# Kernel tuning notes

Hardware: AMD Instinct MI355X
Metric: run time of the kernel (lower is better)

The kernel has to match this reference:

```python
import jax, jax.numpy as jnp
import numpy as np

K_HOPS = 10
ALPHA = 0.1
N_NODES = 50000
N_EDGES = 600000
F_IN = 128
HIDDEN = 64
N_CLASSES = 40


def setup_inputs() -> dict:
    key = jax.random.key(0)
    k1, k2, k3, k4 = jax.random.split(key, 4)
    x = jax.random.normal(k1, (N_NODES, F_IN), dtype=jnp.float32)
    edge_index = jax.random.randint(k2, (2, N_EDGES), 0, N_NODES, dtype=jnp.int32)
    edge_weight = jnp.ones((N_EDGES,), dtype=jnp.float32)
    W1 = jax.random.normal(k3, (F_IN, HIDDEN), dtype=jnp.float32) * (1.0 / np.sqrt(F_IN))
    b1 = jnp.zeros((HIDDEN,), dtype=jnp.float32)
    W2 = jax.random.normal(k4, (HIDDEN, N_CLASSES), dtype=jnp.float32) * (1.0 / np.sqrt(HIDDEN))
    b2 = jnp.zeros((N_CLASSES,), dtype=jnp.float32)
    return {"x": x, "edge_index": edge_index, "edge_weight": edge_weight,
            "W1": W1, "b1": b1, "W2": W2, "b2": b2}


def reference(x, edge_index, edge_weight, W1, b1, W2, b2):
    n = x.shape[0]
    # GCN symmetric normalization with self-loops (tfg gcn cache)
    self_idx = jnp.arange(n, dtype=edge_index.dtype)
    row = jnp.concatenate([edge_index[0], self_idx])
    col = jnp.concatenate([edge_index[1], self_idx])
    w = jnp.concatenate([edge_weight, jnp.ones((n,), dtype=edge_weight.dtype)])
    deg = jax.ops.segment_sum(w, row, num_segments=n)
    dinv = jnp.where(deg > 0, jax.lax.rsqrt(jnp.maximum(deg, 1e-12)), 0.0)
    nw = dinv[row] * w * dinv[col]  # [E+N] normalized edge weights

    def prop(h):
        # h_out[i] = sum_{(i,j)} nw * h[j]
        return jax.ops.segment_sum(h[col] * nw[:, None], row, num_segments=n)

    def step(h, _):
        h_next = prop(h)
        return h_next, None

    # SSGC: out = (1-alpha)/K * sum_{l=1..K} T^l x + alpha * x
    def step_acc(carry, _):
        h, acc = carry
        h_next = prop(h)
        return (h_next, acc + h_next), None

    (_, acc), _ = jax.lax.scan(step_acc, (x, jnp.zeros_like(x)), None, length=K_HOPS)
    h = (1.0 - ALPHA) / K_HOPS * acc + ALPHA * x  # [N, F]

    h = jax.nn.relu(h @ W1 + b1)  # [N, HIDDEN]
    logits = h @ W2 + b2          # [N, N_CLASSES]
    return logits
```

## Files before the change

### kernel.cpp

```cpp
#include <hip/hip_runtime.h>
#include <hip/hip_fp16.h>
#include <math.h>

constexpr int   N   = 50000;
constexpr int   E   = 600000;
constexpr int   FIN = 128;
constexpr int   H   = 64;
constexpr int   C   = 40;
constexpr int   K   = 10;
constexpr float CK  = (1.0f - 0.1f) / 10.0f;
constexpr float AL  = 0.1f;

typedef float v2f __attribute__((ext_vector_type(2)));

__device__ __forceinline__ unsigned pack_fp8x4(float f0, float f1, float f2, float f3) {
    unsigned r = __builtin_amdgcn_cvt_pk_fp8_f32(f0, f1, 0u, false);
    r = __builtin_amdgcn_cvt_pk_fp8_f32(f2, f3, r, true);
    return r;
}

__device__ __forceinline__ float ep_w(unsigned v) {
    return __half2float(__ushort_as_half((unsigned short)(v >> 16)));
}
__device__ __forceinline__ unsigned ep_pack(int c, float w) {
    return (unsigned)(unsigned short)c |
           ((unsigned)__half_as_ushort(__float2half_rn(w)) << 16);
}

__device__ __forceinline__ void accum8(float* s, uint2 v, float w) {
    v2f p0 = __builtin_amdgcn_cvt_pk_f32_fp8(v.x, false);
    v2f p1 = __builtin_amdgcn_cvt_pk_f32_fp8(v.x, true);
    v2f p2 = __builtin_amdgcn_cvt_pk_f32_fp8(v.y, false);
    v2f p3 = __builtin_amdgcn_cvt_pk_f32_fp8(v.y, true);
    s[0] = fmaf(w, p0.x, s[0]); s[1] = fmaf(w, p0.y, s[1]);
    s[2] = fmaf(w, p1.x, s[2]); s[3] = fmaf(w, p1.y, s[3]);
    s[4] = fmaf(w, p2.x, s[4]); s[5] = fmaf(w, p2.y, s[5]);
    s[6] = fmaf(w, p3.x, s[6]); s[7] = fmaf(w, p3.y, s[7]);
}

constexpr int G1N  = 64;
constexpr int XPAD = 132;
__global__ __launch_bounds__(256, 2) void k_gemm1(const float* __restrict__ x,
                                                  const float* __restrict__ W1,
                                                  float* __restrict__ y0,
                                                  unsigned char* __restrict__ y0f8) {
    __shared__ float ws[FIN * H];
    __shared__ float xs[G1N * XPAD];
    const float4* W14 = (const float4*)W1;
    const float4* x4  = (const float4*)x;
    int t = threadIdx.x;
    int node0 = blockIdx.x * G1N;
    for (int i = t; i < FIN * H / 4; i += 256) ((float4*)ws)[i] = W14[i];
    for (int p = 0; p < 8; ++p) {
        int idx = p * 256 + t;
        int n   = idx >> 5;
        int kk  = idx & 31;
        int node = node0 + n;
        float4 v = (node < N) ? x4[(size_t)node * (FIN / 4) + kk]
                              : make_float4(0.f, 0.f, 0.f, 0.f);
        *(float4*)(xs + n * XPAD + kk * 4) = v;
    }
    __syncthreads();
    int nb = (t >> 4) * 4;
    int cb = (t & 15) * 4;
    float a00=0,a01=0,a02=0,a03=0, a10=0,a11=0,a12=0,a13=0;
    float a20=0,a21=0,a22=0,a23=0, a30=0,a31=0,a32=0,a33=0;
#pragma unroll 8
    for (int k = 0; k < FIN; ++k) {
        float4 wv = *(const float4*)(ws + k * H + cb);
        float x0 = xs[(nb + 0) * XPAD + k];
        float x1 = xs[(nb + 1) * XPAD + k];
        float x2 = xs[(nb + 2) * XPAD + k];
        float x3 = xs[(nb + 3) * XPAD + k];
        a00 = fmaf(x0, wv.x, a00); a01 = fmaf(x0, wv.y, a01);
        a02 = fmaf(x0, wv.z, a02); a03 = fmaf(x0, wv.w, a03);
        a10 = fmaf(x1, wv.x, a10); a11 = fmaf(x1, wv.y, a11);
        a12 = fmaf(x1, wv.z, a12); a13 = fmaf(x1, wv.w, a13);
        a20 = fmaf(x2, wv.x, a20); a21 = fmaf(x2, wv.y, a21);
        a22 = fmaf(x2, wv.z, a22); a23 = fmaf(x2, wv.w, a23);
        a30 = fmaf(x3, wv.x, a30); a31 = fmaf(x3, wv.y, a31);
        a32 = fmaf(x3, wv.z, a32); a33 = fmaf(x3, wv.w, a33);
    }
    float4 rows[4] = {make_float4(a00,a01,a02,a03), make_float4(a10,a11,a12,a13),
                      make_float4(a20,a21,a22,a23), make_float4(a30,a31,a32,a33)};
#pragma unroll
    for (int i = 0; i < 4; ++i) {
        int node = node0 + nb + i;
        if (node >= N) break;
        float4 r = rows[i];
        *(float4*)(y0 + (size_t)node * H + cb) = r;
        *(unsigned*)(y0f8 + (size_t)node * H + cb) = pack_fp8x4(r.x, r.y, r.z, r.w);
    }
}

__global__ void k_count(const int* __restrict__ row, int* __restrict__ cnt8) {
    int e = blockIdx.x * blockDim.x + threadIdx.x;
    if (e >= E) return;
    atomicAdd(&cnt8[(size_t)(blockIdx.x & 7) * N + row[e]], 1);
}

__global__ __launch_bounds__(1024) void k_scan_blocks(const int* __restrict__ cnt8,
                                                      int* __restrict__ row_ptr,
                                                      int* __restrict__ bsum) {
    __shared__ int s[1024];
    int gid = blockIdx.x * 1024 + threadIdx.x;
    int v = 0;
    if (gid < N) {
#pragma unroll
        for (int c = 0; c < 8; ++c) v += cnt8[(size_t)c * N + gid];
    }
    s[threadIdx.x] = v;
    __syncthreads();
    for (int off = 1; off < 1024; off <<= 1) {
        int t = (threadIdx.x >= off) ? s[threadIdx.x - off] : 0;
        __syncthreads();
        s[threadIdx.x] += t;
        __syncthreads();
    }
    if (gid < N) row_ptr[gid] = s[threadIdx.x] - v;
    if (threadIdx.x == 1023) bsum[blockIdx.x] = s[1023];
}

__global__ void k_scan_sums(const int* __restrict__ bsum, int* __restrict__ boff, int nb) {
    int lane = threadIdx.x;
    int orig = (lane < nb) ? bsum[lane] : 0;
    int v = orig;
    for (int off = 1; off < 64; off <<= 1) {
        int t = __shfl_up(v, off, 64);
        if (lane >= off) v += t;
    }
    if (lane < nb) boff[lane] = v - orig;
}

__global__ __launch_bounds__(1024) void k_addoff(int* __restrict__ row_ptr,
                                                 const int* __restrict__ boff,
                                                 int* __restrict__ cnt8) {
    int gid = blockIdx.x * 1024 + threadIdx.x;
    if (gid < N) {
        int rp = row_ptr[gid] + boff[blockIdx.x];
        row_ptr[gid] = rp;
        int off = rp;
#pragma unroll
        for (int c = 0; c < 8; ++c) {
            int t = cnt8[(size_t)c * N + gid];
            cnt8[(size_t)c * N + gid] = off;
            off += t;
        }
    }
    if (gid == 0) row_ptr[N] = E;
}

__global__ void k_scatter(const int* __restrict__ row, const int* __restrict__ col,
                          const float* __restrict__ w,
                          int* __restrict__ off8, unsigned* __restrict__ ep) {
    int e = blockIdx.x * blockDim.x + threadIdx.x;
    if (e >= E) return;
    int r = row[e];
    int p = atomicAdd(&off8[(size_t)(blockIdx.x & 7) * N + r], 1);
    ep[p] = ep_pack(col[e], w[e]);
}

__global__ void k_deg_dinv(const unsigned* __restrict__ ep, const int* __restrict__ row_ptr,
                           float* __restrict__ dinv, float* __restrict__ dinv2) {
    int i = blockIdx.x * blockDim.x + threadIdx.x;
    if (i >= N) return;
    float d = 1.0f;
    int e0 = row_ptr[i], e1 = row_ptr[i + 1];
    for (int j = e0; j < e1; ++j) d += ep_w(ep[j]);
    float di = rsqrtf(d);
    dinv[i]  = di;
    dinv2[i] = di * di;
}

__global__ __launch_bounds__(256) void k_norm(unsigned* __restrict__ ep,
                                              const int* __restrict__ row_ptr,
                                              const float* __restrict__ dinv) {
    int node = blockIdx.x * 32 + (threadIdx.x >> 3);
    if (node >= N) return;
    int l = threadIdx.x & 7;
    float dr = dinv[node];
    int e0 = row_ptr[node], e1 = row_ptr[node + 1];
    for (int j = e0 + l; j < e1; j += 8) {
        unsigned v = ep[j];
        int c = v & 0xFFFFu;
        ep[j] = ep_pack(c, ep_w(v) * dr * dinv[c]);
    }
}

constexpr int HSP = 68;
template <bool WRITE_H, bool ACC_INIT, bool FINAL>
__global__ __launch_bounds__(256) void k_prop(const uint2* __restrict__ hin,
                                              uint2* __restrict__ hout,
                                              __half* __restrict__ acch,
                                              const float* __restrict__ dinv2,
                                              const int* __restrict__ row_ptr,
                                              const unsigned* __restrict__ ep,
                                              const float4* __restrict__ y04,
                                              const float* __restrict__ b1,
                                              const float* __restrict__ W2,
                                              const float* __restrict__ b2,
                                              float* __restrict__ out) {
    extern __shared__ float smem[];
    float* w2s = smem;
    float* hs  = smem + H * C;
    float* b2s = hs + 32 * HSP;
    float* b1s = b2s + C;
    int t = threadIdx.x;
    if (FINAL) {
        for (int i = t; i < H * C; i += 256) w2s[i] = W2[i];
        if (t < C) b2s[t] = b2[t];
        if (t < H) b1s[t] = b1[t];
        __syncthreads();
    }
    int lane = t & 63;
    int nib  = (t >> 6) * 8 + (lane >> 3);
    int l    = lane & 7;
    int node = blockIdx.x * 32 + nib;
    bool nv  = node < N;
    int nodec = nv ? node : N - 1;
    int start = row_ptr[nodec];
    int deg   = nv ? (row_ptr[nodec + 1] - start) : 0;
    int md = deg;
#pragma unroll
    for (int off = 8; off <= 32; off <<= 1) md = max(md, __shfl_xor(md, off, 64));
    float s[8];
#pragma unroll
    for (int i = 0; i < 8; ++i) s[i] = 0.f;
    for (int j = 0; j < md; j += 4) {
        bool a0 = j < deg, a1 = j + 1 < deg, a2 = j + 2 < deg, a3 = j + 3 < deg;
        unsigned e0 = ep[a0 ? start + j     : 0];
        unsigned e1 = ep[a1 ? start + j + 1 : 0];
        unsigned e2 = ep[a2 ? start + j + 2 : 0];
        unsigned e3 = ep[a3 ? start + j + 3 : 0];
        uint2 v0 = hin[(size_t)(e0 & 0xFFFFu) * 8 + l];
        uint2 v1 = hin[(size_t)(e1 & 0xFFFFu) * 8 + l];
        uint2 v2 = hin[(size_t)(e2 & 0xFFFFu) * 8 + l];
        uint2 v3 = hin[(size_t)(e3 & 0xFFFFu) * 8 + l];
        accum8(s, v0, a0 ? ep_w(e0) : 0.0f);
        accum8(s, v1, a1 ? ep_w(e1) : 0.0f);
        accum8(s, v2, a2 ? ep_w(e2) : 0.0f);
        accum8(s, v3, a3 ? ep_w(e3) : 0.0f);
    }
    if (nv) {
        size_t base = (size_t)nodec * 8 + l;
        accum8(s, hin[base], dinv2[nodec]);
        if (WRITE_H) {
            uint2 o;
            o.x = pack_fp8x4(s[0], s[1], s[2], s[3]);
            o.y = pack_fp8x4(s[4], s[5], s[6], s[7]);
            hout[base] = o;
        }
        uint4* ap = (uint4*)(acch + (size_t)nodec * H + l * 8);
        if (FINAL) {
            uint4 old = *ap;
            const unsigned* u = (const unsigned*)&old;
#pragma unroll
            for (int d = 0; d < 4; ++d) {
                float2 f = __half22float2(*(__half2*)&u[d]);
                s[2*d+0] += f.x; s[2*d+1] += f.y;
            }
            float4 ya = y04[(size_t)nodec * (H / 4) + 2 * l];
            float4 yb = y04[(size_t)nodec * (H / 4) + 2 * l + 1];
            const float* bp = b1s + l * 8;
            float* hp = hs + nib * HSP + l * 8;
            hp[0] = fmaxf(fmaf(CK, s[0], fmaf(AL, ya.x, bp[0])), 0.f);
            hp[1] = fmaxf(fmaf(CK, s[1], fmaf(AL, ya.y, bp[1])), 0.f);
            hp[2] = fmaxf(fmaf(CK, s[2], fmaf(AL, ya.z, bp[2])), 0.f);
            hp[3] = fmaxf(fmaf(CK, s[3], fmaf(AL, ya.w, bp[3])), 0.f);
            hp[4] = fmaxf(fmaf(CK, s[4], fmaf(AL, yb.x, bp[4])), 0.f);
            hp[5] = fmaxf(fmaf(CK, s[5], fmaf(AL, yb.y, bp[5])), 0.f);
            hp[6] = fmaxf(fmaf(CK, s[6], fmaf(AL, yb.z, bp[6])), 0.f);
            hp[7] = fmaxf(fmaf(CK, s[7], fmaf(AL, yb.w, bp[7])), 0.f);
        } else {
            if (!ACC_INIT) {
                uint4 old = *ap;
                const unsigned* u = (const unsigned*)&old;
#pragma unroll
                for (int d = 0; d < 4; ++d) {
                    float2 f = __half22float2(*(__half2*)&u[d]);
                    s[2*d+0] += f.x; s[2*d+1] += f.y;
                }
            }
            uint4 nvp;
            unsigned* u = (unsigned*)&nvp;
#pragma unroll
            for (int d = 0; d < 4; ++d) {
                __half2 h = __floats2half2_rn(s[2*d+0], s[2*d+1]);
                u[d] = *(unsigned*)&h;
            }
            *ap = nvp;
        }
    }
    if (FINAL) {
        __syncthreads();
        int node0 = blockIdx.x * 32;
        for (int o = t; o < 32 * C; o += 256) {
            int nl = o / C, c = o % C;
            int n2 = node0 + nl;
            if (n2 >= N) continue;
            float v = b2s[c];
            const float* hr = &hs[nl * HSP];
#pragma unroll
            for (int k = 0; k < H; ++k) v = fmaf(hr[k], w2s[k * C + c], v);
            out[n2 * C + c] = v;
        }
    }
}

extern "C" void kernel_launch(void* const* d_in, const int* in_sizes, int n_in,
                              void* d_out, int out_size, void* d_ws, size_t ws_size,
                              hipStream_t stream) {
    const float* x  = (const float*)d_in[0];
    const int*   ei = (const int*)d_in[1];
    const float* ew = (const float*)d_in[2];
    const float* W1 = (const float*)d_in[3];
    const float* b1 = (const float*)d_in[4];
    const float* W2 = (const float*)d_in[5];
    const float* b2 = (const float*)d_in[6];
    float* out = (float*)d_out;

    const int* row = ei;
    const int* col = ei + E;

    char* ws = (char*)d_ws;
    size_t off = 0;
    auto alloc = [&](size_t bytes) -> char* {
        char* p = ws + off;
        off = (off + bytes + 1023) & ~(size_t)1023;
        return p;
    };
    float*         y0   = (float*)alloc((size_t)N * H * 4);
    unsigned char* y0f8 = (unsigned char*)alloc((size_t)N * H);
    unsigned char* ha   = (unsigned char*)alloc((size_t)N * H);
    unsigned char* hb   = (unsigned char*)alloc((size_t)N * H);
    __half*        acch = (__half*)alloc((size_t)N * H * 2);
    int*      cnt8   = (int*)     alloc((size_t)8 * N * 4);
    float*    dinv   = (float*)   alloc((size_t)N * 4);
    float*    dinv2  = (float*)   alloc((size_t)N * 4);
    int*      row_ptr= (int*)     alloc((size_t)(N + 1) * 4);
    int*      bsum   = (int*)     alloc(64 * 4);
    int*      boff   = (int*)     alloc(64 * 4);
    unsigned* ep     = (unsigned*)alloc((size_t)E * 4);

    hipMemsetAsync(cnt8, 0, (size_t)8 * N * 4, stream);

    k_gemm1<<<(N + G1N - 1) / G1N, 256, 0, stream>>>(x, W1, y0, y0f8);

    k_count<<<(E + 255) / 256, 256, 0, stream>>>(row, cnt8);

    constexpr int NB = (N + 1023) / 1024;
    k_scan_blocks<<<NB, 1024, 0, stream>>>(cnt8, row_ptr, bsum);
    k_scan_sums<<<1, 64, 0, stream>>>(bsum, boff, NB);
    k_addoff<<<NB, 1024, 0, stream>>>(row_ptr, boff, cnt8);

    k_scatter<<<(E + 255) / 256, 256, 0, stream>>>(row, col, ew, cnt8, ep);
    k_deg_dinv<<<(N + 255) / 256, 256, 0, stream>>>(ep, row_ptr, dinv, dinv2);
    k_norm<<<(N + 31) / 32, 256, 0, stream>>>(ep, row_ptr, dinv);

    const uint2* hin = (const uint2*)y0f8;
    uint2* bufs[2] = {(uint2*)ha, (uint2*)hb};
    const float4* y04 = (const float4*)y0;
    int grid = (N + 31) / 32;
    size_t smemF = (size_t)(H * C + 32 * HSP + C + H) * 4;
    for (int hop = 0; hop < K; ++hop) {
        uint2* hout = bufs[hop & 1];
        if (hop == 0)
            k_prop<true, true, false><<<grid, 256, 0, stream>>>(hin, hout, acch, dinv2,
                row_ptr, ep, y04, b1, W2, b2, out);
        else if (hop == K - 1)
            k_prop<false, false, true><<<grid, 256, smemF, stream>>>(hin, hout, acch, dinv2,
                row_ptr, ep, y04, b1, W2, b2, out);
        else
            k_prop<true, false, false><<<grid, 256, 0, stream>>>(hin, hout, acch, dinv2,
                row_ptr, ep, y04, b1, W2, b2, out);
        hin = hout;
    }
}
```

Before: 315.6 us.

## Sort nodes by degree to balance per-wavefront work in propagation

Adds a histogram, scan and permutation pass that orders nodes by descending degree (capped at 255). Each propagation kernel then processes nodes through this permutation, so the eight nodes sharing a wavefront have similar degree. That cuts the idle lanes caused by looping to the maximum degree in the group. In exchange, output, accumulator and feature accesses become scattered rather than contiguous, and three small kernels plus a memset are added.

Measured after the change: 640.1 us. 103% more time.

```diff
diff --git a/kernel.cpp b/kernel.cpp
--- a/kernel.cpp
+++ b/kernel.cpp
@@ -187,6 +187,37 @@
     }
 }
 
+__global__ void k_dhist(const int* __restrict__ row_ptr, int* __restrict__ hist) {
+    int i = blockIdx.x * blockDim.x + threadIdx.x;
+    if (i >= N) return;
+    int d = row_ptr[i + 1] - row_ptr[i];
+    atomicAdd(&hist[255 - min(d, 255)], 1);
+}
+
+__global__ __launch_bounds__(256) void k_dscan(int* __restrict__ hist) {
+    __shared__ int s[256];
+    int t = threadIdx.x;
+    int orig = hist[t];
+    s[t] = orig;
+    __syncthreads();
+    for (int off = 1; off < 256; off <<= 1) {
+        int v = (t >= off) ? s[t - off] : 0;
+        __syncthreads();
+        s[t] += v;
+        __syncthreads();
+    }
+    hist[t] = s[t] - orig;
+}
+
+__global__ void k_dperm(const int* __restrict__ row_ptr, int* __restrict__ hist,
+                        int* __restrict__ perm) {
+    int i = blockIdx.x * blockDim.x + threadIdx.x;
+    if (i >= N) return;
+    int d = row_ptr[i + 1] - row_ptr[i];
+    int p = atomicAdd(&hist[255 - min(d, 255)], 1);
+    perm[p] = i;
+}
+
 constexpr int HSP = 68;
 template <bool WRITE_H, bool ACC_INIT, bool FINAL>
 __global__ __launch_bounds__(256) void k_prop(const uint2* __restrict__ hin,
@@ -195,6 +226,7 @@
                                               const float* __restrict__ dinv2,
                                               const int* __restrict__ row_ptr,
                                               const unsigned* __restrict__ ep,
+                                              const int* __restrict__ perm,
                                               const float4* __restrict__ y04,
                                               const float* __restrict__ b1,
                                               const float* __restrict__ W2,
@@ -205,19 +237,20 @@
     float* hs  = smem + H * C;
     float* b2s = hs + 32 * HSP;
     float* b1s = b2s + C;
+    __shared__ int pn[32];
     int t = threadIdx.x;
     if (FINAL) {
         for (int i = t; i < H * C; i += 256) w2s[i] = W2[i];
         if (t < C) b2s[t] = b2[t];
         if (t < H) b1s[t] = b1[t];
-        __syncthreads();
     }
     int lane = t & 63;
     int nib  = (t >> 6) * 8 + (lane >> 3);
     int l    = lane & 7;
-    int node = blockIdx.x * 32 + nib;
-    bool nv  = node < N;
-    int nodec = nv ? node : N - 1;
+    int nid  = blockIdx.x * 32 + nib;
+    bool nv  = nid < N;
+    int nodec = nv ? perm[nid] : (N - 1);
+    if (FINAL && l == 0) pn[nib] = nv ? nodec : -1;
     int start = row_ptr[nodec];
     int deg   = nv ? (row_ptr[nodec + 1] - start) : 0;
     int md = deg;
@@ -293,11 +326,10 @@
     }
     if (FINAL) {
         __syncthreads();
-        int node0 = blockIdx.x * 32;
         for (int o = t; o < 32 * C; o += 256) {
             int nl = o / C, c = o % C;
-            int n2 = node0 + nl;
-            if (n2 >= N) continue;
+            int n2 = pn[nl];
+            if (n2 < 0) continue;
             float v = b2s[c];
             const float* hr = &hs[nl * HSP];
 #pragma unroll
@@ -340,9 +372,12 @@
     int*      row_ptr= (int*)     alloc((size_t)(N + 1) * 4);
     int*      bsum   = (int*)     alloc(64 * 4);
     int*      boff   = (int*)     alloc(64 * 4);
+    int*      hist   = (int*)     alloc(256 * 4);
+    int*      perm   = (int*)     alloc((size_t)N * 4);
     unsigned* ep     = (unsigned*)alloc((size_t)E * 4);
 
     hipMemsetAsync(cnt8, 0, (size_t)8 * N * 4, stream);
+    hipMemsetAsync(hist, 0, 256 * 4, stream);
 
     k_gemm1<<<(N + G1N - 1) / G1N, 256, 0, stream>>>(x, W1, y0, y0f8);
 
@@ -352,6 +387,10 @@
     k_scan_blocks<<<NB, 1024, 0, stream>>>(cnt8, row_ptr, bsum);
     k_scan_sums<<<1, 64, 0, stream>>>(bsum, boff, NB);
     k_addoff<<<NB, 1024, 0, stream>>>(row_ptr, boff, cnt8);
+
+    k_dhist<<<(N + 255) / 256, 256, 0, stream>>>(row_ptr, hist);
+    k_dscan<<<1, 256, 0, stream>>>(hist);
+    k_dperm<<<(N + 255) / 256, 256, 0, stream>>>(row_ptr, hist, perm);
 
     k_scatter<<<(E + 255) / 256, 256, 0, stream>>>(row, col, ew, cnt8, ep);
     k_deg_dinv<<<(N + 255) / 256, 256, 0, stream>>>(ep, row_ptr, dinv, dinv2);
@@ -366,13 +405,13 @@
         uint2* hout = bufs[hop & 1];
         if (hop == 0)
             k_prop<true, true, false><<<grid, 256, 0, stream>>>(hin, hout, acch, dinv2,
-                row_ptr, ep, y04, b1, W2, b2, out);
+                row_ptr, ep, perm, y04, b1, W2, b2, out);
         else if (hop == K - 1)
             k_prop<false, false, true><<<grid, 256, smemF, stream>>>(hin, hout, acch, dinv2,
-                row_ptr, ep, y04, b1, W2, b2, out);
+                row_ptr, ep, perm, y04, b1, W2, b2, out);
         else
             k_prop<true, false, false><<<grid, 256, 0, stream>>>(hin, hout, acch, dinv2,
-                row_ptr, ep, y04, b1, W2, b2, out);
+                row_ptr, ep, perm, y04, b1, W2, b2, out);
         hin = hout;
     }
 }
```

## Pad CSR rows to multiples of four and prefetch edges as uint4

Applied to the files above, without the earlier changes.

Row lengths in the CSR are rounded up to a multiple of four, and the edge array is padded and zero-filled so padded slots hold weight zero and column zero. The propagation kernel then loads four packed edges at once with a single 16-byte load and prefetches the next batch ahead of the gathers. It also hoists the accumulator read before the gather loop to overlap its latency. The cost is a larger edge buffer, an extra memset, and up to three dummy edges per row, which add wasted gathers of node zero's features.

Measured after the change: 322.7 us. +2.2%, slower.

```diff
diff --git a/kernel.cpp b/kernel.cpp
--- a/kernel.cpp
+++ b/kernel.cpp
@@ -108,6 +108,7 @@
     if (gid < N) {
 #pragma unroll
         for (int c = 0; c < 8; ++c) v += cnt8[(size_t)c * N + gid];
+        v = (v + 3) & ~3;
     }
     s[threadIdx.x] = v;
     __syncthreads();
@@ -121,7 +122,8 @@
     if (threadIdx.x == 1023) bsum[blockIdx.x] = s[1023];
 }
 
-__global__ void k_scan_sums(const int* __restrict__ bsum, int* __restrict__ boff, int nb) {
+__global__ void k_scan_sums(const int* __restrict__ bsum, int* __restrict__ boff, int nb,
+                            int* __restrict__ rowN) {
     int lane = threadIdx.x;
     int orig = (lane < nb) ? bsum[lane] : 0;
     int v = orig;
@@ -130,6 +132,7 @@
         if (lane >= off) v += t;
     }
     if (lane < nb) boff[lane] = v - orig;
+    if (lane == nb - 1) *rowN = v;
 }
 
 __global__ __launch_bounds__(1024) void k_addoff(int* __restrict__ row_ptr,
@@ -147,7 +150,6 @@
             off += t;
         }
     }
-    if (gid == 0) row_ptr[N] = E;
 }
 
 __global__ void k_scatter(const int* __restrict__ row, const int* __restrict__ col,
@@ -219,27 +221,36 @@
     bool nv  = node < N;
     int nodec = nv ? node : N - 1;
     int start = row_ptr[nodec];
-    int deg   = nv ? (row_ptr[nodec + 1] - start) : 0;
-    int md = deg;
+    int pdeg  = nv ? (row_ptr[nodec + 1] - start) : 0;
+    int md = pdeg;
 #pragma unroll
     for (int off = 8; off <= 32; off <<= 1) md = max(md, __shfl_xor(md, off, 64));
+
+    uint4* ap = (uint4*)(acch + (size_t)nodec * H + l * 8);
+    uint4 old;
+    if (nv && (FINAL || !ACC_INIT)) old = *ap;
+
     float s[8];
 #pragma unroll
     for (int i = 0; i < 8; ++i) s[i] = 0.f;
-    for (int j = 0; j < md; j += 4) {
-        bool a0 = j < deg, a1 = j + 1 < deg, a2 = j + 2 < deg, a3 = j + 3 < deg;
-        unsigned e0 = ep[a0 ? start + j     : 0];
-        unsigned e1 = ep[a1 ? start + j + 1 : 0];
-        unsigned e2 = ep[a2 ? start + j + 2 : 0];
-        unsigned e3 = ep[a3 ? start + j + 3 : 0];
-        uint2 v0 = hin[(size_t)(e0 & 0xFFFFu) * 8 + l];
-        uint2 v1 = hin[(size_t)(e1 & 0xFFFFu) * 8 + l];
-        uint2 v2 = hin[(size_t)(e2 & 0xFFFFu) * 8 + l];
-        uint2 v3 = hin[(size_t)(e3 & 0xFFFFu) * 8 + l];
-        accum8(s, v0, a0 ? ep_w(e0) : 0.0f);
-        accum8(s, v1, a1 ? ep_w(e1) : 0.0f);
-        accum8(s, v2, a2 ? ep_w(e2) : 0.0f);
-        accum8(s, v3, a3 ? ep_w(e3) : 0.0f);
+
+    const unsigned* rp = ep + start;
+    uint4 e4 = *(const uint4*)rp;
+    for (int batch = 0; batch < md; batch += 4) {
+        uint4 cur = e4;
+        int nb4  = batch + 4;
+        int off4 = (nb4 < pdeg) ? nb4 : 0;
+        e4 = *(const uint4*)(rp + off4);
+        bool a0 = batch     < pdeg, a1 = batch + 1 < pdeg;
+        bool a2 = batch + 2 < pdeg, a3 = batch + 3 < pdeg;
+        uint2 v0 = hin[(size_t)(cur.x & 0xFFFFu) * 8 + l];
+        uint2 v1 = hin[(size_t)(cur.y & 0xFFFFu) * 8 + l];
+        uint2 v2 = hin[(size_t)(cur.z & 0xFFFFu) * 8 + l];
+        uint2 v3 = hin[(size_t)(cur.w & 0xFFFFu) * 8 + l];
+        accum8(s, v0, a0 ? ep_w(cur.x) : 0.0f);
+        accum8(s, v1, a1 ? ep_w(cur.y) : 0.0f);
+        accum8(s, v2, a2 ? ep_w(cur.z) : 0.0f);
+        accum8(s, v3, a3 ? ep_w(cur.w) : 0.0f);
     }
     if (nv) {
         size_t base = (size_t)nodec * 8 + l;
@@ -250,9 +261,7 @@
             o.y = pack_fp8x4(s[4], s[5], s[6], s[7]);
             hout[base] = o;
         }
-        uint4* ap = (uint4*)(acch + (size_t)nodec * H + l * 8);
         if (FINAL) {
-            uint4 old = *ap;
             const unsigned* u = (const unsigned*)&old;
 #pragma unroll
             for (int d = 0; d < 4; ++d) {
@@ -273,7 +282,6 @@
             hp[7] = fmaxf(fmaf(CK, s[7], fmaf(AL, yb.w, bp[7])), 0.f);
         } else {
             if (!ACC_INIT) {
-                uint4 old = *ap;
                 const unsigned* u = (const unsigned*)&old;
 #pragma unroll
                 for (int d = 0; d < 4; ++d) {
@@ -329,6 +337,7 @@
         off = (off + bytes + 1023) & ~(size_t)1023;
         return p;
     };
+    constexpr size_t EPAD = (size_t)E + 3 * (size_t)N + 1024;
     float*         y0   = (float*)alloc((size_t)N * H * 4);
     unsigned char* y0f8 = (unsigned char*)alloc((size_t)N * H);
     unsigned char* ha   = (unsigned char*)alloc((size_t)N * H);
@@ -340,9 +349,10 @@
     int*      row_ptr= (int*)     alloc((size_t)(N + 1) * 4);
     int*      bsum   = (int*)     alloc(64 * 4);
     int*      boff   = (int*)     alloc(64 * 4);
-    unsigned* ep     = (unsigned*)alloc((size_t)E * 4);
+    unsigned* ep     = (unsigned*)alloc(EPAD * 4);
 
     hipMemsetAsync(cnt8, 0, (size_t)8 * N * 4, stream);
+    hipMemsetAsync(ep, 0, EPAD * 4, stream);
 
     k_gemm1<<<(N + G1N - 1) / G1N, 256, 0, stream>>>(x, W1, y0, y0f8);
 
@@ -350,7 +360,7 @@
 
     constexpr int NB = (N + 1023) / 1024;
     k_scan_blocks<<<NB, 1024, 0, stream>>>(cnt8, row_ptr, bsum);
-    k_scan_sums<<<1, 64, 0, stream>>>(bsum, boff, NB);
+    k_scan_sums<<<1, 64, 0, stream>>>(bsum, boff, NB, row_ptr + N);
     k_addoff<<<NB, 1024, 0, stream>>>(row_ptr, boff, cnt8);
 
     k_scatter<<<(E + 255) / 256, 256, 0, stream>>>(row, col, ew, cnt8, ep);
```
